# Performance work log

Measured on AMD Instinct MI355X. Metric: run time of the kernel, lower is better.

## Reference

```python
import jax, jax.numpy as jnp
import numpy as np

HID = 256
POS_FREQ = 10
DIR_FREQ = 4
POS_ENC = 3 * (2 * POS_FREQ + 1)   # 63
DIR_ENC = 3 * (2 * DIR_FREQ + 1)   # 27
N_PTS = 262144


def _posenc(x, num_freq):
    freqs = (2.0 ** jnp.arange(num_freq)).astype(x.dtype)      # [F]
    xf = x[..., None, :] * freqs[:, None]                       # [..., F, D]
    sc = jnp.stack([jnp.sin(xf), jnp.cos(xf)], axis=-2)         # [..., F, 2, D]
    return jnp.concatenate([x, sc.reshape(*x.shape[:-1], -1)], axis=-1)


def _linear_init(key, fan_in, fan_out):
    kw, kb = jax.random.split(key)
    s = 1.0 / np.sqrt(fan_in)
    W = jax.random.uniform(kw, (fan_in, fan_out), jnp.float32, -s, s)
    b = jax.random.uniform(kb, (fan_out,), jnp.float32, -s, s)
    return W, b


def setup_inputs() -> dict:
    key = jax.random.key(0)
    ks = jax.random.split(key, 16)
    inp = {
        "positions": jax.random.normal(ks[0], (N_PTS, 3), jnp.float32),
        "directions": jax.random.normal(ks[1], (N_PTS, 3), jnp.float32),
    }
    W, b = _linear_init(ks[2], POS_ENC, HID)
    inp["W_in"], inp["b_in"] = W, b
    # 7 hidden layers; layer index 4 takes skip concat (HID + POS_ENC)
    for i in range(7):
        fan_in = HID + POS_ENC if i == 4 else HID
        W, b = _linear_init(ks[3 + i], fan_in, HID)
        inp[f"W_h{i}"], inp[f"b_h{i}"] = W, b
    W, b = _linear_init(ks[10], HID, HID + 1)
    inp["W_out"], inp["b_out"] = W, b
    W, b = _linear_init(ks[11], HID + DIR_ENC, HID // 2)
    inp["W_r1"], inp["b_r1"] = W, b
    W, b = _linear_init(ks[12], HID // 2, 3)
    inp["W_r2"], inp["b_r2"] = W, b
    return inp


def _forward(positions, directions, W_in, b_in, hidden_params, W_out, b_out,
             W_r1, b_r1, W_r2, b_r2):
    pe = _posenc(positions, POS_FREQ)    # [N, 63]
    de = _posenc(directions, DIR_FREQ)   # [N, 27]
    h = jax.nn.relu(pe @ W_in + b_in)    # [N, 256]
    for i, (W, b) in enumerate(hidden_params):
        if i == 4:
            h = jnp.concatenate([h, pe], axis=-1)  # skip connection [N, 319]
        h = jax.nn.relu(h @ W + b)
    out = h @ W_out + b_out                      # [N, 257]
    features = out[..., :HID]                    # [N, 256]
    density = jax.nn.relu(out[..., HID:HID + 1])  # [N, 1]
    rgb_in = jnp.concatenate([features, de], axis=-1)  # [N, 283]
    rgb = jax.nn.sigmoid(jax.nn.relu(rgb_in @ W_r1 + b_r1) @ W_r2 + b_r2)  # [N, 3]
    return rgb, density


def reference(positions, directions, W_in, b_in,
              W_h0, b_h0, W_h1, b_h1, W_h2, b_h2, W_h3, b_h3,
              W_h4, b_h4, W_h5, b_h5, W_h6, b_h6,
              W_out, b_out, W_r1, b_r1, W_r2, b_r2):
    hidden = [(W_h0, b_h0), (W_h1, b_h1), (W_h2, b_h2), (W_h3, b_h3),
              (W_h4, b_h4), (W_h5, b_h5), (W_h6, b_h6)]
    return _forward(positions, directions, W_in, b_in, hidden,
                    W_out, b_out, W_r1, b_r1, W_r2, b_r2)
```

## Files before the change

### kernel.cpp

```cpp
#include <hip/hip_runtime.h>
#include <math.h>

#define NPTS 262144
#define MT 64
#define XS 328

typedef __attribute__((ext_vector_type(8))) short bf16x8;
typedef __attribute__((ext_vector_type(4))) float f32x4;
typedef __attribute__((ext_vector_type(2))) unsigned int u32x2;

#if defined(__has_builtin)
#if __has_builtin(__builtin_amdgcn_cvt_pk_bf16_f32)
#define HAVE_CVT_PK_BF16 1
#endif
#endif

__device__ __forceinline__ short f2bf(float f) {
    union { float f; unsigned u; } v; v.f = f;
    unsigned r = v.u + 0x7fffu + ((v.u >> 16) & 1u);
    return (short)(r >> 16);
}
__device__ __forceinline__ unsigned pk2(float a, float b) {
#ifdef HAVE_CVT_PK_BF16
    auto r = __builtin_amdgcn_cvt_pk_bf16_f32(a, b);
    unsigned u; __builtin_memcpy(&u, &r, 4);
    return u;
#else
    return ((unsigned)(unsigned short)f2bf(a)) |
           ((unsigned)(unsigned short)f2bf(b) << 16);
#endif
}

#define OFF_IN   0
#define SZ_IN    (64*256)
#define OFF_H0   (OFF_IN + SZ_IN)
#define SZ_H     (256*256)
#define OFF_H1   (OFF_H0 + SZ_H)
#define OFF_H2   (OFF_H1 + SZ_H)
#define OFF_H3   (OFF_H2 + SZ_H)
#define OFF_H4   (OFF_H3 + SZ_H)
#define SZ_H4    (320*256)
#define OFF_H5   (OFF_H4 + SZ_H4)
#define OFF_H6   (OFF_H5 + SZ_H)
#define OFF_OUT  (OFF_H6 + SZ_H)
#define SZ_OUT   (256*272)
#define OFF_R1   (OFF_OUT + SZ_OUT)
#define SZ_R1    (288*128)
#define OFF_R2   (OFF_R1 + SZ_R1)
#define SZ_R2    (128*16)
#define WS_TOTAL (OFF_R2 + SZ_R2)

struct PrepP { const float* W[11]; short* ws; };

__global__ __launch_bounds__(256) void prep_all(PrepP pp) {
    int i = blockIdx.x * 256 + threadIdx.x;
    if (i >= WS_TOTAL) return;
    const int offs[12] = {OFF_IN, OFF_H0, OFF_H1, OFF_H2, OFF_H3, OFF_H4,
                          OFF_H5, OFF_H6, OFF_OUT, OFF_R1, OFF_R2, WS_TOTAL};
    const int Ks[11]  = {63,256,256,256,256,319,256,256,256,283,128};
    const int Ns[11]  = {256,256,256,256,256,256,256,256,257,128,3};
    const int Nps[11] = {256,256,256,256,256,256,256,256,272,128,16};
    int seg = 0;
    while (i >= offs[seg + 1]) seg++;
    int li = i - offs[seg];
    int j = li & 7, L = (li >> 3) & 63, tile = li >> 9;
    int nNt = Nps[seg] >> 4;
    int nt = tile % nNt, kt = tile / nNt;
    int k = kt * 32 + ((L >> 4) << 3) + j;
    int n = nt * 16 + (L & 15);
    float v = (k < Ks[seg] && n < Ns[seg]) ? pp.W[seg][k * Ns[seg] + n] : 0.f;
    pp.ws[i] = f2bf(v);
}

struct Params {
    const float *pos, *dir;
    const float *b_in, *b_h0, *b_h1, *b_h2, *b_h3, *b_h4, *b_h5, *b_h6;
    const float *b_out, *b_r1, *b_r2;
    const short *w;
    float *out;
};

template<int NKT, int NT, int NS, int TM, int MODE>
__device__ __forceinline__ void layerT(const short* __restrict__ Wsw,
                                       const float* __restrict__ bias,
                                       short* X, float* dout, int p0,
                                       int ntB, int mtB, int wave, int lane) {
    const int l15 = lane & 15, quad = lane >> 4;
    __syncthreads();
    const short* xb = X + l15 * XS + quad * 8;

    if (MODE == 1) {
        f32x4 ad = (f32x4){0.f, 0.f, 0.f, 0.f};
        for (int kt = 0; kt < NKT; ++kt) {
            bf16x8 b = *(const bf16x8*)(xb + wave * 16 * XS + kt * 32);
            bf16x8 a = *(const bf16x8*)(Wsw + (size_t)((kt * NT + 16) * 64 + lane) * 8);
            ad = __builtin_amdgcn_mfma_f32_16x16x32_bf16(a, b, ad, 0, 0, 0);
        }
        if (quad == 0)
            dout[3 * NPTS + p0 + wave * 16 + l15] = fmaxf(ad[0] + bias[256], 0.f);
    }

    f32x4 acc[NS][TM];
#pragma unroll
    for (int s = 0; s < NS; s++)
#pragma unroll
        for (int t = 0; t < TM; t++) acc[s][t] = (f32x4){0.f, 0.f, 0.f, 0.f};

    const short* wp = Wsw + (size_t)((ntB)*64 + lane) * 8;

    bf16x8 a_c[NS], b_c[TM];
#pragma unroll
    for (int s = 0; s < NS; s++)
        a_c[s] = *(const bf16x8*)(wp + (size_t)s * 512);
#pragma unroll
    for (int t = 0; t < TM; t++)
        b_c[t] = *(const bf16x8*)(xb + (mtB + t) * 16 * XS);

#pragma unroll
    for (int kt = 0; kt < NKT; ++kt) {
        bf16x8 a_n[NS], b_n[TM];
        if (kt + 1 < NKT) {
            const short* wp1 = wp + (size_t)(kt + 1) * NT * 512;
#pragma unroll
            for (int s = 0; s < NS; s++)
                a_n[s] = *(const bf16x8*)(wp1 + (size_t)s * 512);
#pragma unroll
            for (int t = 0; t < TM; t++)
                b_n[t] = *(const bf16x8*)(xb + (mtB + t) * 16 * XS + (kt + 1) * 32);
        }
#pragma unroll
        for (int s = 0; s < NS; s++)
#pragma unroll
            for (int t = 0; t < TM; t++)
                acc[s][t] = __builtin_amdgcn_mfma_f32_16x16x32_bf16(a_c[s], b_c[t], acc[s][t], 0, 0, 0);
        if (kt + 1 < NKT) {
#pragma unroll
            for (int s = 0; s < NS; s++) a_c[s] = a_n[s];
#pragma unroll
            for (int t = 0; t < TM; t++) b_c[t] = b_n[t];
        }
    }
    __syncthreads();
#pragma unroll
    for (int s = 0; s < NS; s++) {
        const int n0 = (ntB + s) * 16 + quad * 4;
        const f32x4 bv = *(const f32x4*)(bias + n0);
#pragma unroll
        for (int t = 0; t < TM; t++) {
            const int m = (mtB + t) * 16 + l15;
            float v0 = acc[s][t][0] + bv[0];
            float v1 = acc[s][t][1] + bv[1];
            float v2 = acc[s][t][2] + bv[2];
            float v3 = acc[s][t][3] + bv[3];
            if (MODE == 0) {
                v0 = fmaxf(v0, 0.f); v1 = fmaxf(v1, 0.f);
                v2 = fmaxf(v2, 0.f); v3 = fmaxf(v3, 0.f);
            }
            u32x2 w; w[0] = pk2(v0, v1); w[1] = pk2(v2, v3);
            *(u32x2*)(X + m * XS + n0) = w;
        }
    }
}

__global__ __launch_bounds__(256, 3) void nerf_fused(Params P) {
    __shared__ __align__(16) short X[MT * XS];
    __shared__ __align__(16) short DE[MT * 32];
    const int tid = threadIdx.x;
    const int wave = tid >> 6, lane = tid & 63;
    const int p0 = blockIdx.x * MT;

    const int ntB_h = wave * 4;
    const int ntB_r = wave * 2;

    for (int i = tid; i < MT * 64; i += 256) {
        const int pt = i >> 6, d = i & 63;
        float v = 0.f;
        if (d < 3) v = P.pos[(p0 + pt) * 3 + d];
        else if (d < 63) {
            const int e = d - 3, f = e / 6, r = e % 6;
            const float x = P.pos[(p0 + pt) * 3 + (r % 3)];
            const float xf = x * (float)(1 << f);
            v = (r < 3) ? sinf(xf) : cosf(xf);
        }
        const short bv = f2bf(v);
        X[pt * XS + d] = bv;
        X[pt * XS + 256 + d] = bv;
    }
    for (int i = tid; i < MT * 32; i += 256) {
        const int pt = i >> 5, d = i & 31;
        float v = 0.f;
        if (d < 3) v = P.dir[(p0 + pt) * 3 + d];
        else if (d < 27) {
            const int e = d - 3, f = e / 6, r = e % 6;
            const float x = P.dir[(p0 + pt) * 3 + (r % 3)];
            const float xf = x * (float)(1 << f);
            v = (r < 3) ? sinf(xf) : cosf(xf);
        }
        DE[i] = f2bf(v);
    }

    layerT<2, 16, 4, 4, 0>(P.w + OFF_IN, P.b_in, X, P.out, p0, ntB_h, 0, wave, lane);
    layerT<8, 16, 4, 4, 0>(P.w + OFF_H0, P.b_h0, X, P.out, p0, ntB_h, 0, wave, lane);
    layerT<8, 16, 4, 4, 0>(P.w + OFF_H1, P.b_h1, X, P.out, p0, ntB_h, 0, wave, lane);
    layerT<8, 16, 4, 4, 0>(P.w + OFF_H2, P.b_h2, X, P.out, p0, ntB_h, 0, wave, lane);
    layerT<8, 16, 4, 4, 0>(P.w + OFF_H3, P.b_h3, X, P.out, p0, ntB_h, 0, wave, lane);
    layerT<10, 16, 4, 4, 0>(P.w + OFF_H4, P.b_h4, X, P.out, p0, ntB_h, 0, wave, lane);
    layerT<8, 16, 4, 4, 0>(P.w + OFF_H5, P.b_h5, X, P.out, p0, ntB_h, 0, wave, lane);
    layerT<8, 16, 4, 4, 0>(P.w + OFF_H6, P.b_h6, X, P.out, p0, ntB_h, 0, wave, lane);
    layerT<8, 17, 4, 4, 1>(P.w + OFF_OUT, P.b_out, X, P.out, p0, ntB_h, 0, wave, lane);

    for (int i = tid; i < MT * 32; i += 256) {
        const int pt = i >> 5, d = i & 31;
        X[pt * XS + 256 + d] = DE[i];
    }

    layerT<9, 8, 2, 4, 0>(P.w + OFF_R1, P.b_r1, X, P.out, p0, ntB_r, 0, wave, lane);

    __syncthreads();
    {
        const int l15 = lane & 15, quad = lane >> 4;
        f32x4 acc = (f32x4){0.f, 0.f, 0.f, 0.f};
        const short* xb = X + (wave * 16 + l15) * XS + quad * 8;
#pragma unroll
        for (int kt = 0; kt < 4; ++kt) {
            bf16x8 b = *(const bf16x8*)(xb + kt * 32);
            bf16x8 a = *(const bf16x8*)(P.w + OFF_R2 + (size_t)(kt * 64 + lane) * 8);
            acc = __builtin_amdgcn_mfma_f32_16x16x32_bf16(a, b, acc, 0, 0, 0);
        }
        if (quad == 0) {
#pragma unroll
            for (int r = 0; r < 3; r++) {
                const float v = acc[r] + P.b_r2[r];
                P.out[(size_t)(p0 + wave * 16 + l15) * 3 + r] = 1.f / (1.f + expf(-v));
            }
        }
    }
}

extern "C" void kernel_launch(void* const* d_in, const int* in_sizes, int n_in,
                              void* d_out, int out_size, void* d_ws, size_t ws_size,
                              hipStream_t stream) {
    short* ws = (short*)d_ws;

    PrepP pp;
    pp.W[0]  = (const float*)d_in[2];
    pp.W[1]  = (const float*)d_in[4];
    pp.W[2]  = (const float*)d_in[6];
    pp.W[3]  = (const float*)d_in[8];
    pp.W[4]  = (const float*)d_in[10];
    pp.W[5]  = (const float*)d_in[12];
    pp.W[6]  = (const float*)d_in[14];
    pp.W[7]  = (const float*)d_in[16];
    pp.W[8]  = (const float*)d_in[18];
    pp.W[9]  = (const float*)d_in[20];
    pp.W[10] = (const float*)d_in[22];
    pp.ws = ws;
    hipLaunchKernelGGL(prep_all, dim3((WS_TOTAL + 255) / 256), dim3(256), 0, stream, pp);

    Params P;
    P.pos  = (const float*)d_in[0];
    P.dir  = (const float*)d_in[1];
    P.b_in = (const float*)d_in[3];
    P.b_h0 = (const float*)d_in[5];
    P.b_h1 = (const float*)d_in[7];
    P.b_h2 = (const float*)d_in[9];
    P.b_h3 = (const float*)d_in[11];
    P.b_h4 = (const float*)d_in[13];
    P.b_h5 = (const float*)d_in[15];
    P.b_h6 = (const float*)d_in[17];
    P.b_out = (const float*)d_in[19];
    P.b_r1 = (const float*)d_in[21];
    P.b_r2 = (const float*)d_in[23];
    P.w = ws;
    P.out = (float*)d_out;
    hipLaunchKernelGGL(nerf_fused, dim3(NPTS / MT), dim3(256), 0, stream, P);
}
```

Before: 434.1 us.

## Use k-chunked LDS activation layout and 8 waves per block

Replaces the padded row-major activation buffer with a layout of 8-element k-chunks by point, so MFMA B-operand reads and epilogue writes are contiguous per chunk. Doubles the block to 512 threads, with each wave owning 2 N-tiles instead of 4. This halves per-wave accumulators and raises occupancy (launch bounds 512,4). The direction encoding is now written straight into the skip region after the density layer, which removes the separate DE buffer and its copy. The tradeoff is that each weight fragment is reused across fewer MFMAs per wave, and the density and final RGB layers run on only half the waves.

```diff
diff --git a/kernel.cpp b/kernel.cpp
--- a/kernel.cpp
+++ b/kernel.cpp
@@ -3,7 +3,6 @@
 
 #define NPTS 262144
 #define MT 64
-#define XS 328
 
 typedef __attribute__((ext_vector_type(8))) short bf16x8;
 typedef __attribute__((ext_vector_type(4))) float f32x4;
@@ -80,19 +79,20 @@
     float *out;
 };
 
-template<int NKT, int NT, int NS, int TM, int MODE>
+template<int NKT, int NT, int NS, int MODE>
 __device__ __forceinline__ void layerT(const short* __restrict__ Wsw,
                                        const float* __restrict__ bias,
                                        short* X, float* dout, int p0,
-                                       int ntB, int mtB, int wave, int lane) {
+                                       int ntB, int wave, int lane) {
     const int l15 = lane & 15, quad = lane >> 4;
     __syncthreads();
-    const short* xb = X + l15 * XS + quad * 8;
-
-    if (MODE == 1) {
+    const short* xb = X + quad * 512 + l15 * 8;
+
+    if (MODE == 1 && wave < 4) {
         f32x4 ad = (f32x4){0.f, 0.f, 0.f, 0.f};
+#pragma unroll
         for (int kt = 0; kt < NKT; ++kt) {
-            bf16x8 b = *(const bf16x8*)(xb + wave * 16 * XS + kt * 32);
+            bf16x8 b = *(const bf16x8*)(xb + wave * 128 + kt * 2048);
             bf16x8 a = *(const bf16x8*)(Wsw + (size_t)((kt * NT + 16) * 64 + lane) * 8);
             ad = __builtin_amdgcn_mfma_f32_16x16x32_bf16(a, b, ad, 0, 0, 0);
         }
@@ -100,44 +100,44 @@
             dout[3 * NPTS + p0 + wave * 16 + l15] = fmaxf(ad[0] + bias[256], 0.f);
     }
 
-    f32x4 acc[NS][TM];
+    f32x4 acc[NS][4];
 #pragma unroll
     for (int s = 0; s < NS; s++)
 #pragma unroll
-        for (int t = 0; t < TM; t++) acc[s][t] = (f32x4){0.f, 0.f, 0.f, 0.f};
-
-    const short* wp = Wsw + (size_t)((ntB)*64 + lane) * 8;
-
-    bf16x8 a_c[NS], b_c[TM];
+        for (int t = 0; t < 4; t++) acc[s][t] = (f32x4){0.f, 0.f, 0.f, 0.f};
+
+    const short* wp = Wsw + (size_t)(ntB * 64 + lane) * 8;
+
+    bf16x8 a_c[NS], b_c[4];
 #pragma unroll
     for (int s = 0; s < NS; s++)
         a_c[s] = *(const bf16x8*)(wp + (size_t)s * 512);
 #pragma unroll
-    for (int t = 0; t < TM; t++)
-        b_c[t] = *(const bf16x8*)(xb + (mtB + t) * 16 * XS);
+    for (int t = 0; t < 4; t++)
+        b_c[t] = *(const bf16x8*)(xb + t * 128);
 
 #pragma unroll
     for (int kt = 0; kt < NKT; ++kt) {
-        bf16x8 a_n[NS], b_n[TM];
+        bf16x8 a_n[NS], b_n[4];
         if (kt + 1 < NKT) {
             const short* wp1 = wp + (size_t)(kt + 1) * NT * 512;
 #pragma unroll
             for (int s = 0; s < NS; s++)
                 a_n[s] = *(const bf16x8*)(wp1 + (size_t)s * 512);
 #pragma unroll
-            for (int t = 0; t < TM; t++)
-                b_n[t] = *(const bf16x8*)(xb + (mtB + t) * 16 * XS + (kt + 1) * 32);
+            for (int t = 0; t < 4; t++)
+                b_n[t] = *(const bf16x8*)(xb + (kt + 1) * 2048 + t * 128);
         }
 #pragma unroll
         for (int s = 0; s < NS; s++)
 #pragma unroll
-            for (int t = 0; t < TM; t++)
+            for (int t = 0; t < 4; t++)
                 acc[s][t] = __builtin_amdgcn_mfma_f32_16x16x32_bf16(a_c[s], b_c[t], acc[s][t], 0, 0, 0);
         if (kt + 1 < NKT) {
 #pragma unroll
             for (int s = 0; s < NS; s++) a_c[s] = a_n[s];
 #pragma unroll
-            for (int t = 0; t < TM; t++) b_c[t] = b_n[t];
+            for (int t = 0; t < 4; t++) b_c[t] = b_n[t];
         }
     }
     __syncthreads();
@@ -145,9 +145,10 @@
     for (int s = 0; s < NS; s++) {
         const int n0 = (ntB + s) * 16 + quad * 4;
         const f32x4 bv = *(const f32x4*)(bias + n0);
-#pragma unroll
-        for (int t = 0; t < TM; t++) {
-            const int m = (mtB + t) * 16 + l15;
+        short* xo = X + (2 * (ntB + s) + (quad >> 1)) * 512 + (quad & 1) * 4;
+#pragma unroll
+        for (int t = 0; t < 4; t++) {
+            const int m = t * 16 + l15;
             float v0 = acc[s][t][0] + bv[0];
             float v1 = acc[s][t][1] + bv[1];
             float v2 = acc[s][t][2] + bv[2];
@@ -157,23 +158,21 @@
                 v2 = fmaxf(v2, 0.f); v3 = fmaxf(v3, 0.f);
             }
             u32x2 w; w[0] = pk2(v0, v1); w[1] = pk2(v2, v3);
-            *(u32x2*)(X + m * XS + n0) = w;
-        }
-    }
-}
-
-__global__ __launch_bounds__(256, 3) void nerf_fused(Params P) {
-    __shared__ __align__(16) short X[MT * XS];
-    __shared__ __align__(16) short DE[MT * 32];
+            *(u32x2*)(xo + m * 8) = w;
+        }
+    }
+}
+
+__global__ __launch_bounds__(512, 4) void nerf_fused(Params P) {
+    __shared__ __align__(16) short X[40 * 512];
     const int tid = threadIdx.x;
     const int wave = tid >> 6, lane = tid & 63;
     const int p0 = blockIdx.x * MT;
 
-    const int ntB_h = wave * 4;
-    const int ntB_r = wave * 2;
-
-    for (int i = tid; i < MT * 64; i += 256) {
-        const int pt = i >> 6, d = i & 63;
+    const int ntB_h = wave * 2;
+
+    for (int i = tid; i < MT * 64; i += 512) {
+        const int pt = i & 63, d = i >> 6;
         float v = 0.f;
         if (d < 3) v = P.pos[(p0 + pt) * 3 + d];
         else if (d < 63) {
@@ -183,11 +182,22 @@
             v = (r < 3) ? sinf(xf) : cosf(xf);
         }
         const short bv = f2bf(v);
-        X[pt * XS + d] = bv;
-        X[pt * XS + 256 + d] = bv;
-    }
-    for (int i = tid; i < MT * 32; i += 256) {
-        const int pt = i >> 5, d = i & 31;
+        X[((d >> 3) * 64 + pt) * 8 + (d & 7)] = bv;
+        X[((32 + (d >> 3)) * 64 + pt) * 8 + (d & 7)] = bv;
+    }
+
+    layerT<2, 16, 2, 0>(P.w + OFF_IN, P.b_in, X, P.out, p0, ntB_h, wave, lane);
+    layerT<8, 16, 2, 0>(P.w + OFF_H0, P.b_h0, X, P.out, p0, ntB_h, wave, lane);
+    layerT<8, 16, 2, 0>(P.w + OFF_H1, P.b_h1, X, P.out, p0, ntB_h, wave, lane);
+    layerT<8, 16, 2, 0>(P.w + OFF_H2, P.b_h2, X, P.out, p0, ntB_h, wave, lane);
+    layerT<8, 16, 2, 0>(P.w + OFF_H3, P.b_h3, X, P.out, p0, ntB_h, wave, lane);
+    layerT<10, 16, 2, 0>(P.w + OFF_H4, P.b_h4, X, P.out, p0, ntB_h, wave, lane);
+    layerT<8, 16, 2, 0>(P.w + OFF_H5, P.b_h5, X, P.out, p0, ntB_h, wave, lane);
+    layerT<8, 16, 2, 0>(P.w + OFF_H6, P.b_h6, X, P.out, p0, ntB_h, wave, lane);
+    layerT<8, 17, 2, 1>(P.w + OFF_OUT, P.b_out, X, P.out, p0, ntB_h, wave, lane);
+
+    for (int i = tid; i < MT * 32; i += 512) {
+        const int pt = i & 63, d = i >> 6;
         float v = 0.f;
         if (d < 3) v = P.dir[(p0 + pt) * 3 + d];
         else if (d < 27) {
@@ -196,34 +206,19 @@
             const float xf = x * (float)(1 << f);
             v = (r < 3) ? sinf(xf) : cosf(xf);
         }
-        DE[i] = f2bf(v);
-    }
-
-    layerT<2, 16, 4, 4, 0>(P.w + OFF_IN, P.b_in, X, P.out, p0, ntB_h, 0, wave, lane);
-    layerT<8, 16, 4, 4, 0>(P.w + OFF_H0, P.b_h0, X, P.out, p0, ntB_h, 0, wave, lane);
-    layerT<8, 16, 4, 4, 0>(P.w + OFF_H1, P.b_h1, X, P.out, p0, ntB_h, 0, wave, lane);
-    layerT<8, 16, 4, 4, 0>(P.w + OFF_H2, P.b_h2, X, P.out, p0, ntB_h, 0, wave, lane);
-    layerT<8, 16, 4, 4, 0>(P.w + OFF_H3, P.b_h3, X, P.out, p0, ntB_h, 0, wave, lane);
-    layerT<10, 16, 4, 4, 0>(P.w + OFF_H4, P.b_h4, X, P.out, p0, ntB_h, 0, wave, lane);
-    layerT<8, 16, 4, 4, 0>(P.w + OFF_H5, P.b_h5, X, P.out, p0, ntB_h, 0, wave, lane);
-    layerT<8, 16, 4, 4, 0>(P.w + OFF_H6, P.b_h6, X, P.out, p0, ntB_h, 0, wave, lane);
-    layerT<8, 17, 4, 4, 1>(P.w + OFF_OUT, P.b_out, X, P.out, p0, ntB_h, 0, wave, lane);
-
-    for (int i = tid; i < MT * 32; i += 256) {
-        const int pt = i >> 5, d = i & 31;
-        X[pt * XS + 256 + d] = DE[i];
-    }
-
-    layerT<9, 8, 2, 4, 0>(P.w + OFF_R1, P.b_r1, X, P.out, p0, ntB_r, 0, wave, lane);
+        X[((32 + (d >> 3)) * 64 + pt) * 8 + (d & 7)] = f2bf(v);
+    }
+
+    layerT<9, 8, 1, 0>(P.w + OFF_R1, P.b_r1, X, P.out, p0, wave, wave, lane);
 
     __syncthreads();
-    {
+    if (wave < 4) {
         const int l15 = lane & 15, quad = lane >> 4;
         f32x4 acc = (f32x4){0.f, 0.f, 0.f, 0.f};
-        const short* xb = X + (wave * 16 + l15) * XS + quad * 8;
+        const short* xb = X + quad * 512 + (wave * 16 + l15) * 8;
 #pragma unroll
         for (int kt = 0; kt < 4; ++kt) {
-            bf16x8 b = *(const bf16x8*)(xb + kt * 32);
+            bf16x8 b = *(const bf16x8*)(xb + kt * 2048);
             bf16x8 a = *(const bf16x8*)(P.w + OFF_R2 + (size_t)(kt * 64 + lane) * 8);
             acc = __builtin_amdgcn_mfma_f32_16x16x32_bf16(a, b, acc, 0, 0, 0);
         }
@@ -273,5 +268,5 @@
     P.b_r2 = (const float*)d_in[23];
     P.w = ws;
     P.out = (float*)d_out;
-    hipLaunchKernelGGL(nerf_fused, dim3(NPTS / MT), dim3(256), 0, stream, P);
-}
+    hipLaunchKernelGGL(nerf_fused, dim3(NPTS / MT), dim3(512), 0, stream, P);
+}
```

New measurement: 412.1 us. 1.05x faster.
